# Kernel tuning notes

Hardware: AMD Instinct MI355X
Metric: run time of the kernel (lower is better)

The kernel has to match this reference:

```python
import jax, jax.numpy as jnp
import numpy as np

V, B, T, C, H, L = 32000, 4, 1024, 1024, 16, 8
HS = C // H  # head_size = 64


def _ln(x, g, b):
    m = x.mean(-1, keepdims=True)
    v = x.var(-1, keepdims=True)
    return (x - m) / jnp.sqrt(v + 1e-5) * g + b


def setup_inputs() -> dict:
    key = jax.random.key(0)
    ks = jax.random.split(key, 24)
    s = 0.02
    inp = {
        "idx": jax.random.randint(ks[0], (B, T), 0, V, dtype=jnp.int64),
        "tok_emb": jax.random.normal(ks[1], (V, C), jnp.float32) * s,
        "pos_emb": jax.random.normal(ks[2], (T, C), jnp.float32) * s,
        "Wq": jax.random.normal(ks[3], (L, H, C, HS), jnp.float32) * s,
        "Wk": jax.random.normal(ks[4], (L, H, C, HS), jnp.float32) * s,
        "Wv": jax.random.normal(ks[5], (L, H, C, HS), jnp.float32) * s,
        "Ph_w": jax.random.normal(ks[6], (L, H, HS, C), jnp.float32) * s,
        "Ph_b": jnp.zeros((L, H, C), jnp.float32),
        "Pm_w": jax.random.normal(ks[7], (L, C, C), jnp.float32) * s,
        "Pm_b": jnp.zeros((L, C), jnp.float32),
        "ln1_g": jnp.ones((L, C), jnp.float32),
        "ln1_b": jnp.zeros((L, C), jnp.float32),
        "ln2_g": jnp.ones((L, C), jnp.float32),
        "ln2_b": jnp.zeros((L, C), jnp.float32),
        "W1": jax.random.normal(ks[8], (L, C, 4 * C), jnp.float32) * s,
        "b1": jnp.zeros((L, 4 * C), jnp.float32),
        "W2": jax.random.normal(ks[9], (L, 4 * C, C), jnp.float32) * s,
        "b2": jnp.zeros((L, C), jnp.float32),
        "lnf_g": jnp.ones((C,), jnp.float32),
        "lnf_b": jnp.zeros((C,), jnp.float32),
        "head_w": jax.random.normal(ks[10], (C, V), jnp.float32) * s,
        "head_b": jnp.zeros((V,), jnp.float32),
    }
    return inp


def reference(idx, tok_emb, pos_emb, Wq, Wk, Wv, Ph_w, Ph_b, Pm_w, Pm_b,
              ln1_g, ln1_b, ln2_g, ln2_b, W1, b1, W2, b2, lnf_g, lnf_b,
              head_w, head_b):
    Bx, Tx = idx.shape
    x = tok_emb[idx] + pos_emb[:Tx]  # [B,T,C]
    mask = jnp.tril(jnp.ones((Tx, Tx), bool))
    scale = x.shape[-1] ** -0.5  # NOTE: original scales by n_embd**-0.5, not head_size
    n_layers = Wq.shape[0]
    for l in range(n_layers):
        xn = _ln(x, ln1_g[l], ln1_b[l])
        q = jnp.einsum('btc,hcs->bhts', xn, Wq[l])
        k = jnp.einsum('btc,hcs->bhts', xn, Wk[l])
        v = jnp.einsum('btc,hcs->bhts', xn, Wv[l])
        wei = jnp.einsum('bhts,bhus->bhtu', q, k) * scale
        wei = jnp.where(mask, wei, -jnp.inf)
        wei = jax.nn.softmax(wei, axis=-1)
        o = jnp.einsum('bhtu,bhus->bhts', wei, v)  # [B,H,T,HS]
        per = jnp.einsum('bhts,hsc->bhtc', o, Ph_w[l]) + Ph_b[l][None, :, None, :]
        sa = per.sum(axis=1) @ Pm_w[l] + Pm_b[l]  # combine heads, final proj
        x = x + sa
        xn2 = _ln(x, ln2_g[l], ln2_b[l])
        h = jax.nn.gelu(xn2 @ W1[l] + b1[l], approximate=False)
        x = x + h @ W2[l] + b2[l]
    x = _ln(x, lnf_g, lnf_b)
    return x @ head_w + head_b  # logits [B,T,V]
```

## Files before the change

### kernel.cpp

```cpp
#include <hip/hip_runtime.h>
#include <hip/hip_bf16.h>
#include <math.h>

static constexpr int V = 32000, B = 4, T = 1024, C = 1024, H = 16, NL = 8, HS = 64;
static constexpr int M = B * T;

typedef __bf16 bf16x8 __attribute__((ext_vector_type(8)));
typedef __bf16 bf16x4 __attribute__((ext_vector_type(4)));
typedef float f32x4 __attribute__((ext_vector_type(4)));

__global__ void k_embed(const int* __restrict__ idx, const float* __restrict__ tok,
                        const float* __restrict__ pos, float* __restrict__ x) {
  int g = blockIdx.x * blockDim.x + threadIdx.x;
  if (g >= M * C / 4) return;
  int c4 = g & 255;
  int bt = g >> 8;
  int t = bt & (T - 1);
  int row = idx[bt];
  float4 tv = *(const float4*)(tok + (size_t)row * C + c4 * 4);
  float4 pv = *(const float4*)(pos + (size_t)t * C + c4 * 4);
  float4 o;
  o.x = tv.x + pv.x; o.y = tv.y + pv.y; o.z = tv.z + pv.z; o.w = tv.w + pv.w;
  *(float4*)(x + (size_t)bt * C + c4 * 4) = o;
}

__global__ __launch_bounds__(256) void k_ln_bf(const float* __restrict__ x, const float* __restrict__ g,
                                               const float* __restrict__ b, __hip_bfloat16* __restrict__ y) {
  int row = blockIdx.x, tid = threadIdx.x;
  float4 v = ((const float4*)(x + (size_t)row * C))[tid];
  float s = v.x + v.y + v.z + v.w;
  float ss = v.x * v.x + v.y * v.y + v.z * v.z + v.w * v.w;
  for (int off = 32; off > 0; off >>= 1) {
    s += __shfl_down(s, off);
    ss += __shfl_down(ss, off);
  }
  __shared__ float sb[4], qb[4];
  int wid = tid >> 6;
  if ((tid & 63) == 0) { sb[wid] = s; qb[wid] = ss; }
  __syncthreads();
  float st = sb[0] + sb[1] + sb[2] + sb[3];
  float qt = qb[0] + qb[1] + qb[2] + qb[3];
  float mean = st * (1.0f / C);
  float var = qt * (1.0f / C) - mean * mean;
  float rstd = rsqrtf(var + 1e-5f);
  float4 gv = ((const float4*)g)[tid];
  float4 bv = ((const float4*)b)[tid];
  union { __hip_bfloat16 h[4]; ushort4 u; } pk;
  pk.h[0] = __float2bfloat16((v.x - mean) * rstd * gv.x + bv.x);
  pk.h[1] = __float2bfloat16((v.y - mean) * rstd * gv.y + bv.y);
  pk.h[2] = __float2bfloat16((v.z - mean) * rstd * gv.z + bv.z);
  pk.h[3] = __float2bfloat16((v.w - mean) * rstd * gv.w + bv.w);
  *(ushort4*)(y + (size_t)row * C + tid * 4) = pk.u;
}

__global__ __launch_bounds__(256) void k_transp(const float* __restrict__ in, __hip_bfloat16* __restrict__ out,
                                                int K, int N) {
  __shared__ float t[64][65];
  int n0 = blockIdx.x * 64, k0 = blockIdx.y * 64;
  int tx = threadIdx.x & 15, ty = threadIdx.x >> 4;
#pragma unroll
  for (int i = 0; i < 64; i += 16) {
    float4 v = *(const float4*)(in + (size_t)(k0 + ty + i) * N + n0 + tx * 4);
    t[ty + i][tx * 4 + 0] = v.x;
    t[ty + i][tx * 4 + 1] = v.y;
    t[ty + i][tx * 4 + 2] = v.z;
    t[ty + i][tx * 4 + 3] = v.w;
  }
  __syncthreads();
#pragma unroll
  for (int i = 0; i < 64; i += 16) {
    int n = ty + i;
    union { __hip_bfloat16 h[4]; ushort4 u; } pk;
#pragma unroll
    for (int j = 0; j < 4; ++j) pk.h[j] = __float2bfloat16(t[tx * 4 + j][n]);
    *(ushort4*)(out + (size_t)(n0 + n) * K + k0 + tx * 4) = pk.u;
  }
}

__global__ __launch_bounds__(256) void k_prep_qkv(const float* __restrict__ Wq, const float* __restrict__ Wk,
                                                  const float* __restrict__ Wv, __hip_bfloat16* __restrict__ out) {
  int z = blockIdx.y;
  int sel = z >> 4, h = z & 15;
  const float* W = sel == 0 ? Wq : (sel == 1 ? Wk : Wv);
  const float* in = W + (size_t)h * C * HS;
  __hip_bfloat16* o = out + ((size_t)sel * 1024 + h * 64) * C;
  __shared__ float t[64][65];
  int k0 = blockIdx.x * 64;
  int tx = threadIdx.x & 15, ty = threadIdx.x >> 4;
#pragma unroll
  for (int i = 0; i < 64; i += 16) {
    float4 v = *(const float4*)(in + (size_t)(k0 + ty + i) * HS + tx * 4);
    t[ty + i][tx * 4 + 0] = v.x;
    t[ty + i][tx * 4 + 1] = v.y;
    t[ty + i][tx * 4 + 2] = v.z;
    t[ty + i][tx * 4 + 3] = v.w;
  }
  __syncthreads();
#pragma unroll
  for (int i = 0; i < 64; i += 16) {
    int n = ty + i;
    union { __hip_bfloat16 h4[4]; ushort4 u; } pk;
#pragma unroll
    for (int j = 0; j < 4; ++j) pk.h4[j] = __float2bfloat16(t[tx * 4 + j][n]);
    *(ushort4*)(o + (size_t)n * C + k0 + tx * 4) = pk.u;
  }
}

__global__ void k_bsum(const float* __restrict__ phb, float* __restrict__ bs) {
  int c = blockIdx.x * blockDim.x + threadIdx.x;
  if (c < C) {
    float s = 0.0f;
    for (int h = 0; h < H; ++h) s += phb[(size_t)h * C + c];
    bs[c] = s;
  }
}

template <int BIAS, int GELU, int RES, int OUTBF>
__global__ __launch_bounds__(256) void k_gemm_bf(const __hip_bfloat16* __restrict__ A,
                                                 const __hip_bfloat16* __restrict__ Bt,
                                                 void* Cout, const float* __restrict__ bias,
                                                 const float* res, int N, int K) {
  __shared__ __align__(16) __hip_bfloat16 As[128 * 32];
  __shared__ __align__(16) __hip_bfloat16 Bs[128 * 32];
  int bm = blockIdx.y * 128, bn = blockIdx.x * 128;
  int tid = threadIdx.x;
  int w = tid >> 6, l = tid & 63;
  int wr = (w >> 1) * 64, wc = (w & 1) * 64;
  int lr = l >> 2;
  int lk = (l & 3) * 8;
  int fr = l & 15;
  int fk = (l >> 4) * 8;
  const __hip_bfloat16* Ag = A + (size_t)bm * K;
  const __hip_bfloat16* Bg = Bt + (size_t)bn * K;
  f32x4 acc[4][4];
#pragma unroll
  for (int m = 0; m < 4; ++m)
#pragma unroll
    for (int n = 0; n < 4; ++n) acc[m][n] = (f32x4){0.f, 0.f, 0.f, 0.f};

  for (int k0 = 0; k0 < K; k0 += 32) {
    __syncthreads();
#pragma unroll
    for (int i = 0; i < 2; ++i) {
      int seg = w * 2 + i;
      int r = seg * 16 + lr;
      __builtin_amdgcn_global_load_lds(
          (const __attribute__((address_space(1))) void*)(Ag + (size_t)r * K + k0 + lk),
          (__attribute__((address_space(3))) void*)(As + seg * 512), 16, 0, 0);
      __builtin_amdgcn_global_load_lds(
          (const __attribute__((address_space(1))) void*)(Bg + (size_t)r * K + k0 + lk),
          (__attribute__((address_space(3))) void*)(Bs + seg * 512), 16, 0, 0);
    }
    __syncthreads();
    bf16x8 af[4], bfr[4];
#pragma unroll
    for (int m = 0; m < 4; ++m) af[m] = *(const bf16x8*)(As + ((size_t)(wr + m * 16 + fr)) * 32 + fk);
#pragma unroll
    for (int n = 0; n < 4; ++n) bfr[n] = *(const bf16x8*)(Bs + ((size_t)(wc + n * 16 + fr)) * 32 + fk);
#pragma unroll
    for (int m = 0; m < 4; ++m)
#pragma unroll
      for (int n = 0; n < 4; ++n)
        acc[m][n] = __builtin_amdgcn_mfma_f32_16x16x32_bf16(af[m], bfr[n], acc[m][n], 0, 0, 0);
  }
  int crow0 = (l >> 4) * 4;
  int ccol = l & 15;
#pragma unroll
  for (int m = 0; m < 4; ++m) {
    int row = bm + wr + m * 16 + crow0;
#pragma unroll
    for (int n = 0; n < 4; ++n) {
      int col = bn + wc + n * 16 + ccol;
      float bv = BIAS ? bias[col] : 0.0f;
#pragma unroll
      for (int r = 0; r < 4; ++r) {
        float v = acc[m][n][r] + bv;
        if (GELU) v = 0.5f * v * (1.0f + erff(v * 0.70710678118f));
        if (RES) v += res[(size_t)(row + r) * N + col];
        if (OUTBF)
          ((__hip_bfloat16*)Cout)[(size_t)(row + r) * N + col] = __float2bfloat16(v);
        else
          ((float*)Cout)[(size_t)(row + r) * N + col] = v;
      }
    }
  }
}

__global__ __launch_bounds__(256) void k_attn(const __hip_bfloat16* __restrict__ qkvh,
                                              __hip_bfloat16* __restrict__ o) {
  const __bf16* qkv = (const __bf16*)qkvh;
  int qi = blockIdx.x;
  int bh = blockIdx.y;
  int b = bh >> 4, h = bh & 15;
  int tid = threadIdx.x;
  int w = tid >> 6, l = tid & 63;
  int fr = l & 15, fg = l >> 4;
  int qb = qi * 64;
  int qw = qb + w * 16;

  __shared__ __align__(16) __bf16 Ks[32][72];
  __shared__ __align__(16) __bf16 Vs[32][76];
  __shared__ __align__(16) __bf16 Ps[4][16][40];

  const size_t bT = (size_t)b * T;
  bf16x8 a_q[2];
  {
    const __bf16* qp = qkv + (bT + qw + fr) * 3072 + h * 64 + fg * 8;
    a_q[0] = *(const bf16x8*)qp;
    a_q[1] = *(const bf16x8*)(qp + 32);
  }
  f32x4 acc_o[4];
#pragma unroll
  for (int n = 0; n < 4; ++n) acc_o[n] = (f32x4){0.f, 0.f, 0.f, 0.f};
  float mrow[4] = {-1e30f, -1e30f, -1e30f, -1e30f};
  float lrow[4] = {0.f, 0.f, 0.f, 0.f};

  int sr = tid >> 3;
  int sc = (tid & 7) * 8;
  int ntile = (qi + 1) * 2;
  for (int t = 0; t < ntile; ++t) {
    int kv0 = t * 32;
    __syncthreads();
    {
      const __bf16* kp = qkv + (bT + kv0 + sr) * 3072 + 1024 + h * 64 + sc;
      bf16x8 k8 = *(const bf16x8*)kp;
      bf16x8 v8 = *(const bf16x8*)(kp + 1024);
      *(bf16x8*)&Ks[sr][sc] = k8;
      *(bf16x4*)&Vs[sr][sc] = __builtin_shufflevector(v8, v8, 0, 1, 2, 3);
      *(bf16x4*)&Vs[sr][sc + 4] = __builtin_shufflevector(v8, v8, 4, 5, 6, 7);
    }
    __syncthreads();
    if (kv0 > qw + 15) continue;

    f32x4 s0 = (f32x4){0.f, 0.f, 0.f, 0.f}, s1 = s0;
    s0 = __builtin_amdgcn_mfma_f32_16x16x32_bf16(a_q[0], *(const bf16x8*)&Ks[fr][fg * 8], s0, 0, 0, 0);
    s0 = __builtin_amdgcn_mfma_f32_16x16x32_bf16(a_q[1], *(const bf16x8*)&Ks[fr][32 + fg * 8], s0, 0, 0, 0);
    s1 = __builtin_amdgcn_mfma_f32_16x16x32_bf16(a_q[0], *(const bf16x8*)&Ks[16 + fr][fg * 8], s1, 0, 0, 0);
    s1 = __builtin_amdgcn_mfma_f32_16x16x32_bf16(a_q[1], *(const bf16x8*)&Ks[16 + fr][32 + fg * 8], s1, 0, 0, 0);

    int qrow = qw + fg * 4;
#pragma unroll
    for (int r = 0; r < 4; ++r) { s0[r] *= 0.03125f; s1[r] *= 0.03125f; }
    if (kv0 + 31 > qw) {
#pragma unroll
      for (int r = 0; r < 4; ++r) {
        if (kv0 + fr > qrow + r) s0[r] = -1e30f;
        if (kv0 + 16 + fr > qrow + r) s1[r] = -1e30f;
      }
    }
    float tm[4], psum[4], alpha[4];
#pragma unroll
    for (int r = 0; r < 4; ++r) tm[r] = fmaxf(s0[r], s1[r]);
#pragma unroll
    for (int off = 1; off < 16; off <<= 1)
#pragma unroll
      for (int r = 0; r < 4; ++r) tm[r] = fmaxf(tm[r], __shfl_xor(tm[r], off));
#pragma unroll
    for (int r = 0; r < 4; ++r) {
      float mnew = fmaxf(mrow[r], tm[r]);
      alpha[r] = __expf(mrow[r] - mnew);
      mrow[r] = mnew;
      float p0 = __expf(s0[r] - mnew);
      float p1 = __expf(s1[r] - mnew);
      s0[r] = p0; s1[r] = p1;
      psum[r] = p0 + p1;
    }
#pragma unroll
    for (int off = 1; off < 16; off <<= 1)
#pragma unroll
      for (int r = 0; r < 4; ++r) psum[r] += __shfl_xor(psum[r], off);
#pragma unroll
    for (int r = 0; r < 4; ++r) lrow[r] = lrow[r] * alpha[r] + psum[r];
#pragma unroll
    for (int n = 0; n < 4; ++n)
#pragma unroll
      for (int r = 0; r < 4; ++r) acc_o[n][r] *= alpha[r];

#pragma unroll
    for (int r = 0; r < 4; ++r) {
      Ps[w][fg * 4 + r][fr] = (__bf16)s0[r];
      Ps[w][fg * 4 + r][16 + fr] = (__bf16)s1[r];
    }
    bf16x8 a_p = *(const bf16x8*)&Ps[w][fr][fg * 8];
#pragma unroll
    for (int n = 0; n < 4; ++n) {
      bf16x8 bv;
#pragma unroll
      for (int j = 0; j < 8; ++j) bv[j] = Vs[fg * 8 + j][n * 16 + fr];
      acc_o[n] = __builtin_amdgcn_mfma_f32_16x16x32_bf16(a_p, bv, acc_o[n], 0, 0, 0);
    }
  }
  float inv[4];
#pragma unroll
  for (int r = 0; r < 4; ++r) inv[r] = 1.0f / lrow[r];
  __bf16* ob = (__bf16*)o;
#pragma unroll
  for (int n = 0; n < 4; ++n)
#pragma unroll
    for (int r = 0; r < 4; ++r)
      ob[(bT + qw + fg * 4 + r) * 1024 + h * 64 + n * 16 + fr] = (__bf16)(acc_o[n][r] * inv[r]);
}

extern "C" void kernel_launch(void* const* d_in, const int* in_sizes, int n_in,
                              void* d_out, int out_size, void* d_ws, size_t ws_size,
                              hipStream_t stream) {
  const int* idx = (const int*)d_in[0];
  const float* tok = (const float*)d_in[1];
  const float* pos = (const float*)d_in[2];
  const float* Wq = (const float*)d_in[3];
  const float* Wk = (const float*)d_in[4];
  const float* Wv = (const float*)d_in[5];
  const float* Phw = (const float*)d_in[6];
  const float* Phb = (const float*)d_in[7];
  const float* Pmw = (const float*)d_in[8];
  const float* Pmb = (const float*)d_in[9];
  const float* ln1g = (const float*)d_in[10];
  const float* ln1b = (const float*)d_in[11];
  const float* ln2g = (const float*)d_in[12];
  const float* ln2b = (const float*)d_in[13];
  const float* W1 = (const float*)d_in[14];
  const float* b1 = (const float*)d_in[15];
  const float* W2 = (const float*)d_in[16];
  const float* b2 = (const float*)d_in[17];
  const float* lnfg = (const float*)d_in[18];
  const float* lnfb = (const float*)d_in[19];
  const float* headw = (const float*)d_in[20];
  const float* headb = (const float*)d_in[21];
  float* out = (float*)d_out;

  char* p = (char*)d_ws;
  float* x = (float*)p;                       p += (size_t)M * C * 4;
  float* bsumv = (float*)p;                   p += (size_t)C * 4;
  char* layer_region = p;
  __hip_bfloat16* qkvb = (__hip_bfloat16*)p;  p += (size_t)M * 3072 * 2;
  __hip_bfloat16* ob = (__hip_bfloat16*)p;    p += (size_t)M * C * 2;
  __hip_bfloat16* sa = (__hip_bfloat16*)p;    p += (size_t)M * C * 2;
  __hip_bfloat16* hb = (__hip_bfloat16*)p;    p += (size_t)M * 4 * C * 2;
  __hip_bfloat16* wt = (__hip_bfloat16*)p;    p += (size_t)4 * C * C * 2;
  __hip_bfloat16* xn = (__hip_bfloat16*)p;    p += (size_t)M * C * 2;
  __hip_bfloat16* wt_head = (__hip_bfloat16*)layer_region;

  k_embed<<<(M * C / 4 + 255) / 256, 256, 0, stream>>>(idx, tok, pos, x);

  for (int l = 0; l < NL; ++l) {
    k_ln_bf<<<M, 256, 0, stream>>>(x, ln1g + (size_t)l * C, ln1b + (size_t)l * C, xn);
    k_prep_qkv<<<dim3(16, 48), 256, 0, stream>>>(Wq + (size_t)l * H * C * HS, Wk + (size_t)l * H * C * HS,
                                                 Wv + (size_t)l * H * C * HS, wt);
    k_gemm_bf<0, 0, 0, 1><<<dim3(3072 / 128, M / 128), 256, 0, stream>>>(xn, wt, qkvb, nullptr, nullptr, 3072, C);
    k_attn<<<dim3(T / 64, B * H), 256, 0, stream>>>(qkvb, ob);
    k_bsum<<<(C + 255) / 256, 256, 0, stream>>>(Phb + (size_t)l * H * C, bsumv);
    k_transp<<<dim3(16, 16), 256, 0, stream>>>(Phw + (size_t)l * H * HS * C, wt, C, C);
    k_gemm_bf<1, 0, 0, 1><<<dim3(C / 128, M / 128), 256, 0, stream>>>(ob, wt, sa, bsumv, nullptr, C, C);
    k_transp<<<dim3(16, 16), 256, 0, stream>>>(Pmw + (size_t)l * C * C, wt, C, C);
    k_gemm_bf<1, 0, 1, 0><<<dim3(C / 128, M / 128), 256, 0, stream>>>(sa, wt, x, Pmb + (size_t)l * C, x, C, C);
    k_ln_bf<<<M, 256, 0, stream>>>(x, ln2g + (size_t)l * C, ln2b + (size_t)l * C, xn);
    k_transp<<<dim3(64, 16), 256, 0, stream>>>(W1 + (size_t)l * C * 4 * C, wt, C, 4 * C);
    k_gemm_bf<1, 1, 0, 1><<<dim3(4 * C / 128, M / 128), 256, 0, stream>>>(xn, wt, hb, b1 + (size_t)l * 4 * C, nullptr, 4 * C, C);
    k_transp<<<dim3(16, 64), 256, 0, stream>>>(W2 + (size_t)l * 4 * C * C, wt, 4 * C, C);
    k_gemm_bf<1, 0, 1, 0><<<dim3(C / 128, M / 128), 256, 0, stream>>>(hb, wt, x, b2 + (size_t)l * C, x, C, 4 * C);
  }

  k_ln_bf<<<M, 256, 0, stream>>>(x, lnfg, lnfb, xn);
  k_transp<<<dim3(500, 16), 256, 0, stream>>>(headw, wt_head, C, V);
  k_gemm_bf<1, 0, 0, 0><<<dim3(V / 128, M / 128), 256, 0, stream>>>(xn, wt_head, out, headb, nullptr, V, C);
}
```

Baseline: 3.694 ms.

## Fold head and merge projections into one weight; add 256x256 pipelined GEMM

The per-head output projection and the merge projection are folded into a single weight matrix per layer, computed with a small C×C×C GEMM, and their biases are combined in the same way. This replaces one token-level M×C×C GEMM and its intermediate bf16 buffer with a cheaper weight-only product. It also adds a 256x256-tile, 512-thread GEMM with LDS double buffering, XOR-swizzled shared memory, grid swizzling and priority hints, used for the QKV, FC1 and LM-head GEMMs. The costs are an extra bf16 rounding of the combined weight, a serial bias-combine kernel, and much higher LDS use per block, which limits occupancy.

```diff
diff --git a/kernel.cpp b/kernel.cpp
--- a/kernel.cpp
+++ b/kernel.cpp
@@ -8,6 +8,9 @@
 typedef __bf16 bf16x8 __attribute__((ext_vector_type(8)));
 typedef __bf16 bf16x4 __attribute__((ext_vector_type(4)));
 typedef float f32x4 __attribute__((ext_vector_type(4)));
+
+#define AS1 __attribute__((address_space(1)))
+#define AS3 __attribute__((address_space(3)))
 
 __global__ void k_embed(const int* __restrict__ idx, const float* __restrict__ tok,
                         const float* __restrict__ pos, float* __restrict__ x) {
@@ -77,6 +80,18 @@
   }
 }
 
+__global__ void k_conv(const float* __restrict__ in, __hip_bfloat16* __restrict__ out, int n4) {
+  int g = blockIdx.x * blockDim.x + threadIdx.x;
+  if (g >= n4) return;
+  float4 v = ((const float4*)in)[g];
+  union { __hip_bfloat16 h[4]; ushort4 u; } pk;
+  pk.h[0] = __float2bfloat16(v.x);
+  pk.h[1] = __float2bfloat16(v.y);
+  pk.h[2] = __float2bfloat16(v.z);
+  pk.h[3] = __float2bfloat16(v.w);
+  ((ushort4*)out)[g] = pk.u;
+}
+
 __global__ __launch_bounds__(256) void k_prep_qkv(const float* __restrict__ Wq, const float* __restrict__ Wk,
                                                   const float* __restrict__ Wv, __hip_bfloat16* __restrict__ out) {
   int z = blockIdx.y;
@@ -112,6 +127,16 @@
     float s = 0.0f;
     for (int h = 0; h < H; ++h) s += phb[(size_t)h * C + c];
     bs[c] = s;
+  }
+}
+
+__global__ void k_biascomb(const float* __restrict__ bsum, const float* __restrict__ Pm,
+                           const float* __restrict__ Pmb, float* __restrict__ bc) {
+  int c = blockIdx.x * blockDim.x + threadIdx.x;
+  if (c < C) {
+    float s = Pmb[c];
+    for (int j = 0; j < C; ++j) s += bsum[j] * Pm[(size_t)j * C + c];
+    bc[c] = s;
   }
 }
 
@@ -144,12 +169,10 @@
     for (int i = 0; i < 2; ++i) {
       int seg = w * 2 + i;
       int r = seg * 16 + lr;
-      __builtin_amdgcn_global_load_lds(
-          (const __attribute__((address_space(1))) void*)(Ag + (size_t)r * K + k0 + lk),
-          (__attribute__((address_space(3))) void*)(As + seg * 512), 16, 0, 0);
-      __builtin_amdgcn_global_load_lds(
-          (const __attribute__((address_space(1))) void*)(Bg + (size_t)r * K + k0 + lk),
-          (__attribute__((address_space(3))) void*)(Bs + seg * 512), 16, 0, 0);
+      __builtin_amdgcn_global_load_lds((const AS1 void*)(Ag + (size_t)r * K + k0 + lk),
+                                       (AS3 void*)(As + seg * 512), 16, 0, 0);
+      __builtin_amdgcn_global_load_lds((const AS1 void*)(Bg + (size_t)r * K + k0 + lk),
+                                       (AS3 void*)(Bs + seg * 512), 16, 0, 0);
     }
     __syncthreads();
     bf16x8 af[4], bfr[4];
@@ -186,6 +209,174 @@
   }
 }
 
+template <int BIAS, int GELU, int RES, int OUTBF>
+__global__ __launch_bounds__(512, 2) void k_gemm256(const __hip_bfloat16* __restrict__ Ah,
+                                                    const __hip_bfloat16* __restrict__ Bth,
+                                                    void* Cout, const float* __restrict__ bias,
+                                                    const float* res, int N, int K) {
+  __shared__ __align__(16) __bf16 As[2][256 * 64];
+  __shared__ __align__(16) __bf16 Bs[2][256 * 64];
+  const __bf16* A = (const __bf16*)Ah;
+  const __bf16* Bt = (const __bf16*)Bth;
+  const int nx = N >> 8;
+  const int bid = blockIdx.x;
+  const int sw = ((bid & 7) * ((int)gridDim.x >> 3)) + (bid >> 3);
+  const int bn = (sw % nx) << 8;
+  const int bm = (sw / nx) << 8;
+  const int tid = threadIdx.x, w = tid >> 6, l = tid & 63;
+  const int wm = w >> 2, wn = w & 3;
+  const int fr = l & 15, fg = l >> 4;
+  const int srow = w * 8 + (l >> 3);
+  const int scolb = ((l & 7) * 16) ^ ((l & 32) ? 32 : 0) ^ ((w & 1) ? 16 : 0);
+  const __bf16* Ag = A + (size_t)(bm + srow) * K + (scolb >> 1);
+  const __bf16* Bg = Bt + (size_t)(bn + srow) * K + (scolb >> 1);
+  const int arow = wm * 128 + fr;
+  const int brow = wn * 64 + fr;
+  const int kswz = ((fr & 4) << 3) ^ ((fr & 8) << 1);
+
+  f32x4 acc[8][4];
+#pragma unroll
+  for (int m = 0; m < 8; ++m)
+#pragma unroll
+    for (int n = 0; n < 4; ++n) acc[m][n] = (f32x4){0.f, 0.f, 0.f, 0.f};
+
+  auto stage = [&](int bufi, size_t kel) {
+    const __bf16* ag_ = Ag + kel;
+    const __bf16* bg_ = Bg + kel;
+#pragma unroll
+    for (int jj = 0; jj < 4; ++jj)
+      __builtin_amdgcn_global_load_lds((const AS1 void*)(ag_ + (size_t)jj * 64 * K),
+                                       (AS3 void*)(&As[bufi][jj * 4096 + w * 512]), 16, 0, 0);
+#pragma unroll
+    for (int jj = 0; jj < 4; ++jj)
+      __builtin_amdgcn_global_load_lds((const AS1 void*)(bg_ + (size_t)jj * 64 * K),
+                                       (AS3 void*)(&Bs[bufi][jj * 4096 + w * 512]), 16, 0, 0);
+  };
+
+  const int NT = K >> 6;
+  stage(0, 0);
+  asm volatile("s_waitcnt vmcnt(0)" ::: "memory");
+  __builtin_amdgcn_sched_barrier(0);
+  __builtin_amdgcn_s_barrier();
+  __builtin_amdgcn_sched_barrier(0);
+
+  for (int t = 0; t < NT; ++t) {
+    const int cb = t & 1;
+    const int nb = cb ^ 1;
+    bf16x8 af[4][2], bv[2][2];
+
+#define RD_A(MG, KS) \
+  (*(const bf16x8*)(&As[cb][(arow + (MG) * 16) * 64 + (((((KS) * 64) + fg * 16) ^ kswz) >> 1)]))
+#define RD_B(NG, KS) \
+  (*(const bf16x8*)(&Bs[cb][(brow + (NG) * 16) * 64 + (((((KS) * 64) + fg * 16) ^ kswz) >> 1)]))
+#define BAR() \
+  __builtin_amdgcn_sched_barrier(0); __builtin_amdgcn_s_barrier(); __builtin_amdgcn_sched_barrier(0)
+
+#pragma unroll
+    for (int m = 0; m < 4; ++m) {
+      af[m][0] = RD_A(m, 0);
+      af[m][1] = RD_A(m, 1);
+    }
+#pragma unroll
+    for (int n = 0; n < 2; ++n) {
+      bv[n][0] = RD_B(n, 0);
+      bv[n][1] = RD_B(n, 1);
+    }
+    if (t + 1 < NT) stage(nb, (size_t)(t + 1) * 64);
+    BAR();
+    __builtin_amdgcn_s_setprio(1);
+#pragma unroll
+    for (int m = 0; m < 4; ++m)
+#pragma unroll
+      for (int n = 0; n < 2; ++n)
+#pragma unroll
+        for (int ks = 0; ks < 2; ++ks)
+          acc[m][n] = __builtin_amdgcn_mfma_f32_16x16x32_bf16(af[m][ks], bv[n][ks], acc[m][n], 0, 0, 0);
+    __builtin_amdgcn_s_setprio(0);
+    BAR();
+
+#pragma unroll
+    for (int n = 0; n < 2; ++n) {
+      bv[n][0] = RD_B(2 + n, 0);
+      bv[n][1] = RD_B(2 + n, 1);
+    }
+    BAR();
+    __builtin_amdgcn_s_setprio(1);
+#pragma unroll
+    for (int m = 0; m < 4; ++m)
+#pragma unroll
+      for (int n = 0; n < 2; ++n)
+#pragma unroll
+        for (int ks = 0; ks < 2; ++ks)
+          acc[m][2 + n] = __builtin_amdgcn_mfma_f32_16x16x32_bf16(af[m][ks], bv[n][ks], acc[m][2 + n], 0, 0, 0);
+    __builtin_amdgcn_s_setprio(0);
+    BAR();
+
+#pragma unroll
+    for (int m = 0; m < 4; ++m) {
+      af[m][0] = RD_A(4 + m, 0);
+      af[m][1] = RD_A(4 + m, 1);
+    }
+#pragma unroll
+    for (int n = 0; n < 2; ++n) {
+      bv[n][0] = RD_B(n, 0);
+      bv[n][1] = RD_B(n, 1);
+    }
+    BAR();
+    __builtin_amdgcn_s_setprio(1);
+#pragma unroll
+    for (int m = 0; m < 4; ++m)
+#pragma unroll
+      for (int n = 0; n < 2; ++n)
+#pragma unroll
+        for (int ks = 0; ks < 2; ++ks)
+          acc[4 + m][n] = __builtin_amdgcn_mfma_f32_16x16x32_bf16(af[m][ks], bv[n][ks], acc[4 + m][n], 0, 0, 0);
+    __builtin_amdgcn_s_setprio(0);
+    BAR();
+
+#pragma unroll
+    for (int n = 0; n < 2; ++n) {
+      bv[n][0] = RD_B(2 + n, 0);
+      bv[n][1] = RD_B(2 + n, 1);
+    }
+    BAR();
+    __builtin_amdgcn_s_setprio(1);
+#pragma unroll
+    for (int m = 0; m < 4; ++m)
+#pragma unroll
+      for (int n = 0; n < 2; ++n)
+#pragma unroll
+        for (int ks = 0; ks < 2; ++ks)
+          acc[4 + m][2 + n] = __builtin_amdgcn_mfma_f32_16x16x32_bf16(af[m][ks], bv[n][ks], acc[4 + m][2 + n], 0, 0, 0);
+    __builtin_amdgcn_s_setprio(0);
+    asm volatile("s_waitcnt vmcnt(0)" ::: "memory");
+    BAR();
+#undef RD_A
+#undef RD_B
+#undef BAR
+  }
+
+#pragma unroll
+  for (int mg = 0; mg < 8; ++mg) {
+    int row = bm + wm * 128 + mg * 16 + fg * 4;
+#pragma unroll
+    for (int n = 0; n < 4; ++n) {
+      int col = bn + wn * 64 + n * 16 + fr;
+      float bvx = BIAS ? bias[col] : 0.0f;
+#pragma unroll
+      for (int r = 0; r < 4; ++r) {
+        float v = acc[mg][n][r] + bvx;
+        if (GELU) v = 0.5f * v * (1.0f + erff(v * 0.70710678118f));
+        if (RES) v += res[(size_t)(row + r) * N + col];
+        if (OUTBF)
+          ((__hip_bfloat16*)Cout)[(size_t)(row + r) * N + col] = __float2bfloat16(v);
+        else
+          ((float*)Cout)[(size_t)(row + r) * N + col] = v;
+      }
+    }
+  }
+}
+
 __global__ __launch_bounds__(256) void k_attn(const __hip_bfloat16* __restrict__ qkvh,
                                               __hip_bfloat16* __restrict__ o) {
   const __bf16* qkv = (const __bf16*)qkvh;
@@ -195,8 +386,7 @@
   int tid = threadIdx.x;
   int w = tid >> 6, l = tid & 63;
   int fr = l & 15, fg = l >> 4;
-  int qb = qi * 64;
-  int qw = qb + w * 16;
+  int qw = qi * 64 + w * 16;
 
   __shared__ __align__(16) __bf16 Ks[32][72];
   __shared__ __align__(16) __bf16 Vs[32][76];
@@ -284,10 +474,10 @@
     bf16x8 a_p = *(const bf16x8*)&Ps[w][fr][fg * 8];
 #pragma unroll
     for (int n = 0; n < 4; ++n) {
-      bf16x8 bv;
-#pragma unroll
-      for (int j = 0; j < 8; ++j) bv[j] = Vs[fg * 8 + j][n * 16 + fr];
-      acc_o[n] = __builtin_amdgcn_mfma_f32_16x16x32_bf16(a_p, bv, acc_o[n], 0, 0, 0);
+      bf16x8 bvv;
+#pragma unroll
+      for (int j = 0; j < 8; ++j) bvv[j] = Vs[fg * 8 + j][n * 16 + fr];
+      acc_o[n] = __builtin_amdgcn_mfma_f32_16x16x32_bf16(a_p, bvv, acc_o[n], 0, 0, 0);
     }
   }
   float inv[4];
@@ -330,13 +520,16 @@
 
   char* p = (char*)d_ws;
   float* x = (float*)p;                       p += (size_t)M * C * 4;
-  float* bsumv = (float*)p;                   p += (size_t)C * 4;
+  float* bsumv = (float*)p;                   p += 4096;
+  float* bcv = (float*)p;                     p += 4096;
   char* layer_region = p;
   __hip_bfloat16* qkvb = (__hip_bfloat16*)p;  p += (size_t)M * 3072 * 2;
   __hip_bfloat16* ob = (__hip_bfloat16*)p;    p += (size_t)M * C * 2;
-  __hip_bfloat16* sa = (__hip_bfloat16*)p;    p += (size_t)M * C * 2;
   __hip_bfloat16* hb = (__hip_bfloat16*)p;    p += (size_t)M * 4 * C * 2;
   __hip_bfloat16* wt = (__hip_bfloat16*)p;    p += (size_t)4 * C * C * 2;
+  __hip_bfloat16* wtPmT = (__hip_bfloat16*)p; p += (size_t)C * C * 2;
+  __hip_bfloat16* wtPh = (__hip_bfloat16*)p;  p += (size_t)C * C * 2;
+  __hip_bfloat16* wcombT = (__hip_bfloat16*)p; p += (size_t)C * C * 2;
   __hip_bfloat16* xn = (__hip_bfloat16*)p;    p += (size_t)M * C * 2;
   __hip_bfloat16* wt_head = (__hip_bfloat16*)layer_region;
 
@@ -346,21 +539,22 @@
     k_ln_bf<<<M, 256, 0, stream>>>(x, ln1g + (size_t)l * C, ln1b + (size_t)l * C, xn);
     k_prep_qkv<<<dim3(16, 48), 256, 0, stream>>>(Wq + (size_t)l * H * C * HS, Wk + (size_t)l * H * C * HS,
                                                  Wv + (size_t)l * H * C * HS, wt);
-    k_gemm_bf<0, 0, 0, 1><<<dim3(3072 / 128, M / 128), 256, 0, stream>>>(xn, wt, qkvb, nullptr, nullptr, 3072, C);
+    k_gemm256<0, 0, 0, 1><<<(3072 / 256) * (M / 256), 512, 0, stream>>>(xn, wt, qkvb, nullptr, nullptr, 3072, C);
     k_attn<<<dim3(T / 64, B * H), 256, 0, stream>>>(qkvb, ob);
     k_bsum<<<(C + 255) / 256, 256, 0, stream>>>(Phb + (size_t)l * H * C, bsumv);
-    k_transp<<<dim3(16, 16), 256, 0, stream>>>(Phw + (size_t)l * H * HS * C, wt, C, C);
-    k_gemm_bf<1, 0, 0, 1><<<dim3(C / 128, M / 128), 256, 0, stream>>>(ob, wt, sa, bsumv, nullptr, C, C);
-    k_transp<<<dim3(16, 16), 256, 0, stream>>>(Pmw + (size_t)l * C * C, wt, C, C);
-    k_gemm_bf<1, 0, 1, 0><<<dim3(C / 128, M / 128), 256, 0, stream>>>(sa, wt, x, Pmb + (size_t)l * C, x, C, C);
+    k_transp<<<dim3(16, 16), 256, 0, stream>>>(Pmw + (size_t)l * C * C, wtPmT, C, C);
+    k_conv<<<(C * C / 4 + 255) / 256, 256, 0, stream>>>(Phw + (size_t)l * H * HS * C, wtPh, C * C / 4);
+    k_gemm_bf<0, 0, 0, 1><<<dim3(C / 128, C / 128), 256, 0, stream>>>(wtPmT, wtPh, wcombT, nullptr, nullptr, C, C);
+    k_biascomb<<<(C + 255) / 256, 256, 0, stream>>>(bsumv, Pmw + (size_t)l * C * C, Pmb + (size_t)l * C, bcv);
+    k_gemm_bf<1, 0, 1, 0><<<dim3(C / 128, M / 128), 256, 0, stream>>>(ob, wcombT, x, bcv, x, C, C);
     k_ln_bf<<<M, 256, 0, stream>>>(x, ln2g + (size_t)l * C, ln2b + (size_t)l * C, xn);
     k_transp<<<dim3(64, 16), 256, 0, stream>>>(W1 + (size_t)l * C * 4 * C, wt, C, 4 * C);
-    k_gemm_bf<1, 1, 0, 1><<<dim3(4 * C / 128, M / 128), 256, 0, stream>>>(xn, wt, hb, b1 + (size_t)l * 4 * C, nullptr, 4 * C, C);
+    k_gemm256<1, 1, 0, 1><<<(4 * C / 256) * (M / 256), 512, 0, stream>>>(xn, wt, hb, b1 + (size_t)l * 4 * C, nullptr, 4 * C, C);
     k_transp<<<dim3(16, 64), 256, 0, stream>>>(W2 + (size_t)l * 4 * C * C, wt, 4 * C, C);
     k_gemm_bf<1, 0, 1, 0><<<dim3(C / 128, M / 128), 256, 0, stream>>>(hb, wt, x, b2 + (size_t)l * C, x, C, 4 * C);
   }
 
   k_ln_bf<<<M, 256, 0, stream>>>(x, lnfg, lnfb, xn);
   k_transp<<<dim3(500, 16), 256, 0, stream>>>(headw, wt_head, C, V);
-  k_gemm_bf<1, 0, 0, 0><<<dim3(V / 128, M / 128), 256, 0, stream>>>(xn, wt_head, out, headb, nullptr, V, C);
-}
+  k_gemm256<1, 0, 0, 0><<<(V / 256) * (M / 256), 512, 0, stream>>>(xn, wt_head, out, headb, nullptr, V, C);
+}
```

Result: slower. 4.211 ms (+14.0%).
